# Optimization experiments

Measured on AMD Instinct MI355X. Metric: run time of the kernel, lower is better.

Reference implementation:

```python
import jax, jax.numpy as jnp
import numpy as np

N_NODES = 100000
N_EDGES = 1600000
IN_DIM = 128
OUT_DIM = 128


def setup_inputs() -> dict:
    key = jax.random.key(0)
    k1, k2, k3, k4, k5 = jax.random.split(key, 5)
    x = jax.random.normal(k1, (N_NODES, IN_DIM), dtype=jnp.float32)
    edge_src = jax.random.randint(k2, (N_EDGES,), 0, N_NODES, dtype=jnp.int32)
    edge_dst = jax.random.randint(k3, (N_EDGES,), 0, N_NODES, dtype=jnp.int32)
    # nn.Linear(in_dim*2, out_dim): W stored here as [2*in_dim, out_dim] (already transposed)
    W = jax.random.normal(k4, (2 * IN_DIM, OUT_DIM), dtype=jnp.float32) * (1.0 / np.sqrt(2 * IN_DIM))
    b = jax.random.normal(k5, (OUT_DIM,), dtype=jnp.float32) * 0.01
    return {"x": x, "edge_src": edge_src, "edge_dst": edge_dst, "W": W, "b": b}


def reference(x, edge_src, edge_dst, W, b):
    # adj_mean @ x  ==  mean over neighbors: sum_j x[src_j] into row dst_j, / deg(dst)
    n = x.shape[0]
    deg = jax.ops.segment_sum(jnp.ones_like(edge_dst, dtype=x.dtype), edge_dst, num_segments=n)
    deg = jnp.maximum(deg, 1.0)  # rows with no neighbors -> zero vector (0/1)
    neigh = jax.ops.segment_sum(x[edge_src], edge_dst, num_segments=n) / deg[:, None]
    # concat([x, neigh], dim=1) then Linear
    out = jnp.concatenate([x, neigh], axis=1) @ W + b
    return out
```

## Files before the change

kernel.cpp:

```cpp
#include <hip/hip_runtime.h>

#define IN_DIM 128
#define OUT_DIM 128
#define PADCAP 1792
#define EPB 8192

typedef short bf16x8 __attribute__((ext_vector_type(8)));
typedef float f32x4 __attribute__((ext_vector_type(4)));
typedef float f32x2 __attribute__((ext_vector_type(2)));

__device__ __forceinline__ unsigned short f2bf(float f) {
    union { float f; unsigned int u; } v; v.f = f;
    unsigned int u = v.u;
    u += 0x7FFFu + ((u >> 16) & 1u);
    return (unsigned short)(u >> 16);
}

__global__ __launch_bounds__(1024) void prep_place_kernel(
        const int* __restrict__ src, const int* __restrict__ dst,
        int* __restrict__ cursor, unsigned int* __restrict__ csr_packed,
        const float* __restrict__ x, unsigned char* __restrict__ xq,
        const float* __restrict__ W, unsigned short* __restrict__ WF,
        int nE, int nb, int nN, int total8, int eblk, int qblk) {
    __shared__ int lcnt[2048];
    __shared__ int lbase[2048];
    const int b = blockIdx.x;
    const int t = threadIdx.x;

    if (b < eblk) {
        for (int i = t; i < nb; i += 1024) lcnt[i] = 0;
        __syncthreads();
        const int e0 = b * EPB;
        unsigned int meta[EPB / 1024];
#pragma unroll
        for (int k = 0; k < EPB / 1024; k++) {
            int e = e0 + k * 1024 + t;
            if (e < nE) {
                int d = dst[e];
                int bk = d >> 6, dl = d & 63;
                int r = atomicAdd(&lcnt[bk], 1);
                meta[k] = ((unsigned)bk << 20) | ((unsigned)dl << 14) | (unsigned)r;
            } else meta[k] = 0xFFFFFFFFu;
        }
        __syncthreads();
        for (int i = t; i < nb; i += 1024) {
            int c = lcnt[i];
            lbase[i] = c ? atomicAdd(&cursor[i], c) : 0;
        }
        __syncthreads();
#pragma unroll
        for (int k = 0; k < EPB / 1024; k++) {
            if (meta[k] != 0xFFFFFFFFu) {
                int e = e0 + k * 1024 + t;
                unsigned int m = meta[k];
                int bk = m >> 20, dl = (m >> 14) & 63, r = m & 0x3FFF;
                csr_packed[(size_t)bk * PADCAP + lbase[bk] + r] =
                    ((unsigned)dl << 17) | (unsigned)src[e];
            }
        }
    } else if (b < eblk + qblk) {
        int i = (b - eblk) * 1024 + t;
        if (i >= total8) return;
        const float4* p = (const float4*)x + (size_t)i * 2;
        float4 v0 = p[0], v1 = p[1];
        int w0 = 0, w1 = 0;
        w0 = __builtin_amdgcn_cvt_pk_fp8_f32(v0.x, v0.y, w0, false);
        w0 = __builtin_amdgcn_cvt_pk_fp8_f32(v0.z, v0.w, w0, true);
        w1 = __builtin_amdgcn_cvt_pk_fp8_f32(v1.x, v1.y, w1, false);
        w1 = __builtin_amdgcn_cvt_pk_fp8_f32(v1.z, v1.w, w1, true);
        uint2 o; o.x = (unsigned int)w0; o.y = (unsigned int)w1;
        int node = i >> 4, oct = i & 15;
        int q = oct >> 2, o8 = oct & 3;
        *(uint2*)(xq + (size_t)q * (nN + 1) * 32 + (size_t)node * 32 + o8 * 8) = o;
    } else if (b < eblk + qblk + 4) {
        int tt = (b - eblk - qblk) * 1024 + t;
        int frag = tt >> 6, lane = tt & 63;
        int f = frag >> 3, c = frag & 7;
        int col = c * 16 + (lane & 15);
        int kbase = f * 32 + (lane >> 4) * 8;
        bf16x8 h;
#pragma unroll
        for (int i = 0; i < 8; i++)
            h[i] = (short)f2bf(W[(size_t)(kbase + i) * OUT_DIM + col]);
        *(bf16x8*)(WF + (size_t)tt * 8) = h;
    } else {
        if (t < 32) {
            int q = t >> 3, o = t & 7;
            *(unsigned int*)(xq + (size_t)q * (nN + 1) * 32 + (size_t)nN * 32 + o * 4) = 0u;
        }
    }
}

__global__ __launch_bounds__(256) void sort_kernel(unsigned int* __restrict__ csr_packed,
                                                   const int* __restrict__ cursor,
                                                   unsigned int* __restrict__ rowinfo,
                                                   int nN, int nb) {
    __shared__ int bcnt[64];
    __shared__ int bpst[64];
    __shared__ unsigned int sorted[PADCAP];
    const int b = blockIdx.x;
    const int t = threadIdx.x;
    const int lane = t & 63;
    const int wave = t >> 6;
    const size_t e0 = (size_t)b * PADCAP;
    int n = cursor[b];
    if (n > PADCAP) n = PADCAP;

    const unsigned int sentinel = (unsigned)nN << 5;
    if (t < 64) bcnt[t] = 0;
#pragma unroll
    for (int k = 0; k < 7; k++) sorted[k * 256 + t] = sentinel;
    __syncthreads();

    unsigned int pk[7]; int rk[7];
#pragma unroll
    for (int k = 0; k < 7; k++) {
        int idx = k * 256 + t;
        if (idx < n) {
            unsigned int p = csr_packed[e0 + idx];
            pk[k] = p;
            rk[k] = atomicAdd(&bcnt[(p >> 17) & 63], 1);
        } else pk[k] = 0xFFFFFFFFu;
    }
    __syncthreads();

    if (wave == 0) {
        int dg = bcnt[lane];
        int pl = (dg + 7) & ~7;
        int s = pl;
#pragma unroll
        for (int off = 1; off < 64; off <<= 1) {
            int u = __shfl_up(s, off);
            if (lane >= off) s += u;
        }
        bpst[lane] = s - pl;
    }
    __syncthreads();

#pragma unroll
    for (int k = 0; k < 7; k++) {
        if (pk[k] != 0xFFFFFFFFu) {
            int dl = (pk[k] >> 17) & 63;
            sorted[bpst[dl] + rk[k]] = (pk[k] & 0x1FFFFu) << 5;
        }
    }
    __syncthreads();

#pragma unroll
    for (int k = 0; k < 7; k++) {
        int idx = k * 256 + t;
        csr_packed[e0 + idx] = sorted[idx];
    }
    if (t < 64) rowinfo[b * 64 + t] = (unsigned)bpst[t] | ((unsigned)bcnt[t] << 16);
}

__global__ __launch_bounds__(256, 8) void qgather_kernel(const unsigned char* __restrict__ xq,
                                                         const unsigned int* __restrict__ csr_packed,
                                                         const unsigned int* __restrict__ rowinfo,
                                                         unsigned short* __restrict__ neigh,
                                                         int nN, int nb) {
    __shared__ unsigned int el[PADCAP];
    __shared__ int bst[64];
    __shared__ int bdg[64];

    const int bid = blockIdx.x;
    const int xcd = bid & 7;
    const int quarter = xcd & 3;
    const int bucket = (bid >> 3) * 2 + (xcd >> 2);
    if (bucket >= nb) return;

    const int t = threadIdx.x;
    const int lane = t & 63;
    const int wave = t >> 6;

    if (t < 64) {
        unsigned int ri = rowinfo[bucket * 64 + t];
        bst[t] = (int)(ri & 0xFFFFu);
        bdg[t] = (int)(ri >> 16);
    }
    __syncthreads();
    const size_t e0 = (size_t)bucket * PADCAP;
    const int npad = bst[63] + ((bdg[63] + 7) & ~7);
    for (int idx = t; idx < npad; idx += 256) el[idx] = csr_packed[e0 + idx];
    __syncthreads();

    const unsigned char* plane = xq + (size_t)quarter * (nN + 1) * 32 + (t & 7) * 4;
    const int g = lane >> 3;
    const int c = lane & 7;
    const int qoff = quarter * 32;

#pragma unroll
    for (int set = 0; set < 2; set++) {
        const int r  = wave * 16 + set * 8 + g;
        const int st = bst[r];
        const int dg = bdg[r];
        const int pl = (dg + 7) & ~7;
        f32x2 a0{0.f, 0.f}, a1{0.f, 0.f};
        for (int j = 0; j < pl; j += 8) {
#pragma unroll
            for (int u = 0; u < 8; u++) {
                unsigned int s = el[st + j + u];
                unsigned int v = *(const unsigned int*)(plane + s);
                f32x2 p;
                p = __builtin_amdgcn_cvt_pk_f32_fp8(v, false); a0 += p;
                p = __builtin_amdgcn_cvt_pk_f32_fp8(v, true);  a1 += p;
            }
        }
        const float rd = 1.0f / (float)((dg > 0) ? dg : 1);
        a0 *= rd; a1 *= rd;
        unsigned int w0, w1;
        asm("v_cvt_pk_bf16_f32 %0, %1, %2" : "=v"(w0) : "v"(a0.x), "v"(a0.y));
        asm("v_cvt_pk_bf16_f32 %0, %1, %2" : "=v"(w1) : "v"(a1.x), "v"(a1.y));
        uint2 o; o.x = w0; o.y = w1;
        const int row = bucket * 64 + r;
        *(uint2*)(neigh + (size_t)row * IN_DIM + qoff + c * 4) = o;
    }
}

__global__ __launch_bounds__(256, 6) void gemm_kernel(const float* __restrict__ x,
                                                      const unsigned short* __restrict__ neigh,
                                                      const unsigned short* __restrict__ WF,
                                                      const float* __restrict__ bias,
                                                      float* __restrict__ out, int nN) {
    const int t = threadIdx.x;
    const int lane = t & 63;
    const int wave = t >> 6;
    const int row0 = blockIdx.x * 64;

    f32x4 acc[8];
#pragma unroll
    for (int c = 0; c < 8; c++) acc[c] = f32x4{0.f, 0.f, 0.f, 0.f};

    const int arow = wave * 16 + (lane & 15);
    const int koff = (lane >> 4) * 8;
    const int rowc = min(row0 + arow, nN - 1);
    const float*          xrow = x     + (size_t)rowc * IN_DIM;
    const unsigned short* nrow = neigh + (size_t)rowc * IN_DIM;

#pragma unroll
    for (int f = 0; f < 8; f++) {
        bf16x8 af;
        if (f < 4) {
            const float* px = xrow + f * 32 + koff;
            float4 v0 = *(const float4*)px;
            float4 v1 = *(const float4*)(px + 4);
            unsigned int r0, r1, r2, r3;
            asm("v_cvt_pk_bf16_f32 %0, %1, %2" : "=v"(r0) : "v"(v0.x), "v"(v0.y));
            asm("v_cvt_pk_bf16_f32 %0, %1, %2" : "=v"(r1) : "v"(v0.z), "v"(v0.w));
            asm("v_cvt_pk_bf16_f32 %0, %1, %2" : "=v"(r2) : "v"(v1.x), "v"(v1.y));
            asm("v_cvt_pk_bf16_f32 %0, %1, %2" : "=v"(r3) : "v"(v1.z), "v"(v1.w));
            union { unsigned int u[4]; bf16x8 v; } cv;
            cv.u[0] = r0; cv.u[1] = r1; cv.u[2] = r2; cv.u[3] = r3;
            af = cv.v;
        } else {
            af = *(const bf16x8*)(nrow + (f - 4) * 32 + koff);
        }
#pragma unroll
        for (int c = 0; c < 8; c++) {
            bf16x8 bf = *(const bf16x8*)(WF + ((size_t)(f * 8 + c) * 64 + lane) * 8);
            acc[c] = __builtin_amdgcn_mfma_f32_16x16x32_bf16(af, bf, acc[c], 0, 0, 0);
        }
    }

    const int orow0 = row0 + wave * 16 + (lane >> 4) * 4;
    const int ocol  = lane & 15;
#pragma unroll
    for (int c = 0; c < 8; c++) {
        const float bv = bias[c * 16 + ocol];
#pragma unroll
        for (int r = 0; r < 4; r++) {
            int row = orow0 + r;
            if (row < nN)
                out[(size_t)row * OUT_DIM + c * 16 + ocol] = acc[c][r] + bv;
        }
    }
}

extern "C" void kernel_launch(void* const* d_in, const int* in_sizes, int n_in,
                              void* d_out, int out_size, void* d_ws, size_t ws_size,
                              hipStream_t stream) {
    const float* x        = (const float*)d_in[0];
    const int*   edge_src = (const int*)d_in[1];
    const int*   edge_dst = (const int*)d_in[2];
    const float* W        = (const float*)d_in[3];
    const float* bias     = (const float*)d_in[4];
    float* out = (float*)d_out;

    const int nN = in_sizes[0] / IN_DIM;
    const int nE = in_sizes[1];
    const int nb = (nN + 63) >> 6;

    int* cursor = (int*)d_ws;
    unsigned int* csr_packed = (unsigned int*)(cursor + 2048);
    unsigned int* rowinfo = csr_packed + (size_t)nb * PADCAP;
    unsigned char* xq = (unsigned char*)(rowinfo + (size_t)nb * 64);
    unsigned short* WF = (unsigned short*)(xq + (size_t)4 * (nN + 1) * 32);
    unsigned short* neigh = WF + 128 * 256;

    hipMemsetAsync(cursor, 0, (size_t)nb * sizeof(int), stream);

    const int total8 = nN * IN_DIM / 8;
    const int eblk = (nE + EPB - 1) / EPB;
    const int qblk = (total8 + 1023) / 1024;
    prep_place_kernel<<<eblk + qblk + 4 + 1, 1024, 0, stream>>>(
        edge_src, edge_dst, cursor, csr_packed, x, xq, W, WF,
        nE, nb, nN, total8, eblk, qblk);

    sort_kernel<<<nb, 256, 0, stream>>>(csr_packed, cursor, rowinfo, nN, nb);

    const int nbp2 = (nb + 1) / 2;
    qgather_kernel<<<nbp2 * 8, 256, 0, stream>>>(xq, csr_packed, rowinfo, neigh, nN, nb);
    gemm_kernel<<<(nN + 63) / 64, 256, 0, stream>>>(x, neigh, WF, bias, out, nN);
}
```

Before: 111.2 us.

## Split prep and edge placement into separate kernels, widen gather lanes to 8 bytes

The fused prep/place kernel is split in two. A 256-thread prep kernel converts x to fp8, packs W, and initialises per-bucket cursors to absolute offsets, which replaces the memset. A separate place kernel then scatters edges into the CSR using those absolute cursor values. The gather kernel now has each lane load 8 fp8 bytes instead of 4, so each thread handles one row with four accumulators instead of two rows with two. The cost is an extra kernel launch and serialising the fp8 conversion ahead of edge placement, which previously ran in the same grid.

```diff
diff --git a/kernel.cpp b/kernel.cpp
--- a/kernel.cpp
+++ b/kernel.cpp
@@ -8,6 +8,7 @@
 typedef short bf16x8 __attribute__((ext_vector_type(8)));
 typedef float f32x4 __attribute__((ext_vector_type(4)));
 typedef float f32x2 __attribute__((ext_vector_type(2)));
+typedef unsigned int u32x4 __attribute__((ext_vector_type(4)));
 
 __device__ __forceinline__ unsigned short f2bf(float f) {
     union { float f; unsigned int u; } v; v.f = f;
@@ -16,50 +17,16 @@
     return (unsigned short)(u >> 16);
 }
 
-__global__ __launch_bounds__(1024) void prep_place_kernel(
-        const int* __restrict__ src, const int* __restrict__ dst,
-        int* __restrict__ cursor, unsigned int* __restrict__ csr_packed,
-        const float* __restrict__ x, unsigned char* __restrict__ xq,
-        const float* __restrict__ W, unsigned short* __restrict__ WF,
-        int nE, int nb, int nN, int total8, int eblk, int qblk) {
-    __shared__ int lcnt[2048];
-    __shared__ int lbase[2048];
+__global__ __launch_bounds__(256) void prep_kernel(const float* __restrict__ x,
+                                                   unsigned char* __restrict__ xq,
+                                                   const float* __restrict__ W,
+                                                   unsigned short* __restrict__ WF,
+                                                   int* __restrict__ cursor,
+                                                   int nN, int total8, int nconv, int nb) {
     const int b = blockIdx.x;
     const int t = threadIdx.x;
-
-    if (b < eblk) {
-        for (int i = t; i < nb; i += 1024) lcnt[i] = 0;
-        __syncthreads();
-        const int e0 = b * EPB;
-        unsigned int meta[EPB / 1024];
-#pragma unroll
-        for (int k = 0; k < EPB / 1024; k++) {
-            int e = e0 + k * 1024 + t;
-            if (e < nE) {
-                int d = dst[e];
-                int bk = d >> 6, dl = d & 63;
-                int r = atomicAdd(&lcnt[bk], 1);
-                meta[k] = ((unsigned)bk << 20) | ((unsigned)dl << 14) | (unsigned)r;
-            } else meta[k] = 0xFFFFFFFFu;
-        }
-        __syncthreads();
-        for (int i = t; i < nb; i += 1024) {
-            int c = lcnt[i];
-            lbase[i] = c ? atomicAdd(&cursor[i], c) : 0;
-        }
-        __syncthreads();
-#pragma unroll
-        for (int k = 0; k < EPB / 1024; k++) {
-            if (meta[k] != 0xFFFFFFFFu) {
-                int e = e0 + k * 1024 + t;
-                unsigned int m = meta[k];
-                int bk = m >> 20, dl = (m >> 14) & 63, r = m & 0x3FFF;
-                csr_packed[(size_t)bk * PADCAP + lbase[bk] + r] =
-                    ((unsigned)dl << 17) | (unsigned)src[e];
-            }
-        }
-    } else if (b < eblk + qblk) {
-        int i = (b - eblk) * 1024 + t;
+    if (b < nconv) {
+        int i = b * 256 + t;
         if (i >= total8) return;
         const float4* p = (const float4*)x + (size_t)i * 2;
         float4 v0 = p[0], v1 = p[1];
@@ -72,8 +39,8 @@
         int node = i >> 4, oct = i & 15;
         int q = oct >> 2, o8 = oct & 3;
         *(uint2*)(xq + (size_t)q * (nN + 1) * 32 + (size_t)node * 32 + o8 * 8) = o;
-    } else if (b < eblk + qblk + 4) {
-        int tt = (b - eblk - qblk) * 1024 + t;
+    } else if (b < nconv + 16) {
+        int tt = (b - nconv) * 256 + t;
         int frag = tt >> 6, lane = tt & 63;
         int f = frag >> 3, c = frag & 7;
         int col = c * 16 + (lane & 15);
@@ -83,10 +50,52 @@
         for (int i = 0; i < 8; i++)
             h[i] = (short)f2bf(W[(size_t)(kbase + i) * OUT_DIM + col]);
         *(bf16x8*)(WF + (size_t)tt * 8) = h;
-    } else {
+    } else if (b == nconv + 16) {
         if (t < 32) {
             int q = t >> 3, o = t & 7;
             *(unsigned int*)(xq + (size_t)q * (nN + 1) * 32 + (size_t)nN * 32 + o * 4) = 0u;
+        }
+    } else {
+        int i = (b - nconv - 17) * 256 + t;
+        if (i < nb) cursor[i] = i * PADCAP;
+    }
+}
+
+__global__ __launch_bounds__(1024) void place_kernel(const int* __restrict__ src,
+                                                     const int* __restrict__ dst,
+                                                     int* __restrict__ cursor,
+                                                     unsigned int* __restrict__ csr_packed,
+                                                     int nE, int nb) {
+    __shared__ int lcnt[2048];
+    __shared__ int lbase[2048];
+    const int t = threadIdx.x;
+    for (int i = t; i < nb; i += 1024) lcnt[i] = 0;
+    __syncthreads();
+    const int e0 = blockIdx.x * EPB;
+    unsigned int meta[EPB / 1024];
+#pragma unroll
+    for (int k = 0; k < EPB / 1024; k++) {
+        int e = e0 + k * 1024 + t;
+        if (e < nE) {
+            int d = dst[e];
+            int bk = d >> 6, dl = d & 63;
+            int r = atomicAdd(&lcnt[bk], 1);
+            meta[k] = ((unsigned)bk << 20) | ((unsigned)dl << 14) | (unsigned)r;
+        } else meta[k] = 0xFFFFFFFFu;
+    }
+    __syncthreads();
+    for (int i = t; i < nb; i += 1024) {
+        int c = lcnt[i];
+        lbase[i] = c ? atomicAdd(&cursor[i], c) : 0;
+    }
+    __syncthreads();
+#pragma unroll
+    for (int k = 0; k < EPB / 1024; k++) {
+        if (meta[k] != 0xFFFFFFFFu) {
+            int e = e0 + k * 1024 + t;
+            unsigned int m = meta[k];
+            int bk = m >> 20, dl = (m >> 14) & 63, r = m & 0x3FFF;
+            csr_packed[lbase[bk] + r] = ((unsigned)dl << 17) | (unsigned)src[e];
         }
     }
 }
@@ -103,7 +112,7 @@
     const int lane = t & 63;
     const int wave = t >> 6;
     const size_t e0 = (size_t)b * PADCAP;
-    int n = cursor[b];
+    int n = cursor[b] - (int)e0;
     if (n > PADCAP) n = PADCAP;
 
     const unsigned int sentinel = (unsigned)nN << 5;
@@ -184,37 +193,40 @@
     for (int idx = t; idx < npad; idx += 256) el[idx] = csr_packed[e0 + idx];
     __syncthreads();
 
-    const unsigned char* plane = xq + (size_t)quarter * (nN + 1) * 32 + (t & 7) * 4;
-    const int g = lane >> 3;
-    const int c = lane & 7;
+    const int g = lane >> 2;
+    const int c = lane & 3;
+    const unsigned char* plane = xq + (size_t)quarter * (nN + 1) * 32 + c * 8;
     const int qoff = quarter * 32;
 
-#pragma unroll
-    for (int set = 0; set < 2; set++) {
-        const int r  = wave * 16 + set * 8 + g;
-        const int st = bst[r];
-        const int dg = bdg[r];
-        const int pl = (dg + 7) & ~7;
-        f32x2 a0{0.f, 0.f}, a1{0.f, 0.f};
-        for (int j = 0; j < pl; j += 8) {
-#pragma unroll
-            for (int u = 0; u < 8; u++) {
-                unsigned int s = el[st + j + u];
-                unsigned int v = *(const unsigned int*)(plane + s);
-                f32x2 p;
-                p = __builtin_amdgcn_cvt_pk_f32_fp8(v, false); a0 += p;
-                p = __builtin_amdgcn_cvt_pk_f32_fp8(v, true);  a1 += p;
-            }
-        }
-        const float rd = 1.0f / (float)((dg > 0) ? dg : 1);
-        a0 *= rd; a1 *= rd;
-        unsigned int w0, w1;
-        asm("v_cvt_pk_bf16_f32 %0, %1, %2" : "=v"(w0) : "v"(a0.x), "v"(a0.y));
-        asm("v_cvt_pk_bf16_f32 %0, %1, %2" : "=v"(w1) : "v"(a1.x), "v"(a1.y));
-        uint2 o; o.x = w0; o.y = w1;
-        const int row = bucket * 64 + r;
-        *(uint2*)(neigh + (size_t)row * IN_DIM + qoff + c * 4) = o;
-    }
+    const int r  = wave * 16 + g;
+    const int st = bst[r];
+    const int dg = bdg[r];
+    const int pl = (dg + 7) & ~7;
+    const unsigned int* ep = el + st;
+
+    f32x2 a0{0.f, 0.f}, a1{0.f, 0.f}, a2{0.f, 0.f}, a3{0.f, 0.f};
+    for (int j = 0; j < pl; j += 8) {
+#pragma unroll
+        for (int u = 0; u < 8; u++) {
+            unsigned int s = ep[j + u];
+            uint2 v = *(const uint2*)(plane + s);
+            f32x2 p;
+            p = __builtin_amdgcn_cvt_pk_f32_fp8(v.x, false); a0 += p;
+            p = __builtin_amdgcn_cvt_pk_f32_fp8(v.x, true);  a1 += p;
+            p = __builtin_amdgcn_cvt_pk_f32_fp8(v.y, false); a2 += p;
+            p = __builtin_amdgcn_cvt_pk_f32_fp8(v.y, true);  a3 += p;
+        }
+    }
+    const float rd = 1.0f / (float)((dg > 0) ? dg : 1);
+    a0 *= rd; a1 *= rd; a2 *= rd; a3 *= rd;
+    unsigned int w0, w1, w2, w3;
+    asm("v_cvt_pk_bf16_f32 %0, %1, %2" : "=v"(w0) : "v"(a0.x), "v"(a0.y));
+    asm("v_cvt_pk_bf16_f32 %0, %1, %2" : "=v"(w1) : "v"(a1.x), "v"(a1.y));
+    asm("v_cvt_pk_bf16_f32 %0, %1, %2" : "=v"(w2) : "v"(a2.x), "v"(a2.y));
+    asm("v_cvt_pk_bf16_f32 %0, %1, %2" : "=v"(w3) : "v"(a3.x), "v"(a3.y));
+    u32x4 o = {w0, w1, w2, w3};
+    const int row = bucket * 64 + r;
+    *(u32x4*)(neigh + (size_t)row * IN_DIM + qoff + c * 8) = o;
 }
 
 __global__ __launch_bounds__(256, 6) void gemm_kernel(const float* __restrict__ x,
@@ -297,15 +309,14 @@
     unsigned short* WF = (unsigned short*)(xq + (size_t)4 * (nN + 1) * 32);
     unsigned short* neigh = WF + 128 * 256;
 
-    hipMemsetAsync(cursor, 0, (size_t)nb * sizeof(int), stream);
-
     const int total8 = nN * IN_DIM / 8;
+    const int nconv  = (total8 + 255) / 256;
+    const int ninit  = (nb + 255) / 256;
+    prep_kernel<<<nconv + 17 + ninit, 256, 0, stream>>>(x, xq, W, WF, cursor,
+                                                        nN, total8, nconv, nb);
+
     const int eblk = (nE + EPB - 1) / EPB;
-    const int qblk = (total8 + 1023) / 1024;
-    prep_place_kernel<<<eblk + qblk + 4 + 1, 1024, 0, stream>>>(
-        edge_src, edge_dst, cursor, csr_packed, x, xq, W, WF,
-        nE, nb, nN, total8, eblk, qblk);
-
+    place_kernel<<<eblk, 1024, 0, stream>>>(edge_src, edge_dst, cursor, csr_packed, nE, nb);
     sort_kernel<<<nb, 256, 0, stream>>>(csr_packed, cursor, rowinfo, nN, nb);
 
     const int nbp2 = (nb + 1) / 2;
```

Result: no change. 110.5 us (-0.6%).
